# Performance work log

Measured on AMD Instinct MI355X. Metric: run time of the kernel, lower is better.

## Reference

```python
import jax, jax.numpy as jnp
import numpy as np

EMBED = 1024
HEADS = 16
DIM_HEAD = EMBED // HEADS
N, L = 4, 2048


def setup_inputs() -> dict:
    key = jax.random.key(0)
    ks = jax.random.split(key, 12)
    s = 0.02
    return {
        "q": jax.random.normal(ks[0], (N, L, EMBED), jnp.float32),
        "k": jax.random.normal(ks[1], (N, L, EMBED), jnp.float32),
        "v": jax.random.normal(ks[2], (N, L, EMBED), jnp.float32),
        "padding_mask": jnp.ones((N, L), dtype=bool),
        "sequence_mask": jnp.zeros((L, L), dtype=bool),
        # Linear(in, out): store weight as [out, in] like torch, bias [out]
        "Wq": jax.random.normal(ks[3], (EMBED, EMBED), jnp.float32) * s,
        "bq": jnp.zeros((EMBED,), jnp.float32),
        "Wk": jax.random.normal(ks[4], (EMBED, EMBED), jnp.float32) * s,
        "bk": jnp.zeros((EMBED,), jnp.float32),
        "Wv": jax.random.normal(ks[5], (EMBED, EMBED), jnp.float32) * s,
        "bv": jnp.zeros((EMBED,), jnp.float32),
        "Wo": jax.random.normal(ks[6], (EMBED, EMBED), jnp.float32) * s,
        "bo": jnp.zeros((EMBED,), jnp.float32),
    }


def reference(q, k, v, padding_mask, sequence_mask, Wq, bq, Wk, bk, Wv, bv, Wo, bo):
    n, lq, _ = q.shape
    lk = k.shape[1]
    # input projections
    qp = (q @ Wq.T + bq).reshape(n, lq, HEADS, DIM_HEAD)
    kp = (k @ Wk.T + bk).reshape(n, lk, HEADS, DIM_HEAD)
    vp = (v @ Wv.T + bv).reshape(n, lk, HEADS, DIM_HEAD)
    # energy: [n, h, lq, lk]
    energy = jnp.einsum('nqhd,nkhd->nhqk', qp, kp)
    attention = jax.nn.softmax(energy / jnp.sqrt(jnp.float32(EMBED)), axis=3)
    # NOTE: the original torch code calls masked_fill (non in-place) and
    # discards the result, so padding_mask / sequence_mask have NO effect.
    # Dropout is also never applied in forward. Replicated faithfully.
    out = jnp.einsum('nhqk,nkhd->nqhd', attention, vp)
    out = out.reshape(n, lq, EMBED)
    return out @ Wo.T + bo
```

## Files before the change

### kernel.cpp

```cpp
#include <hip/hip_runtime.h>
#include <stdint.h>

typedef _Float16 f16;
typedef _Float16 f16x8 __attribute__((ext_vector_type(8)));
typedef _Float16 f16x4 __attribute__((ext_vector_type(4)));
typedef _Float16 f16x2 __attribute__((ext_vector_type(2)));
typedef float f32x4 __attribute__((ext_vector_type(4)));

__device__ __forceinline__ f32x4 mfma16(f16x8 a, f16x8 b, f32x4 c) {
    return __builtin_amdgcn_mfma_f32_16x16x32_f16(a, b, c, 0, 0, 0);
}

__device__ __forceinline__ void gload16(const f16* g, f16* l) {
    __builtin_amdgcn_global_load_lds(
        (const __attribute__((address_space(1))) uint32_t*)g,
        (__attribute__((address_space(3))) uint32_t*)l, 16, 0, 0);
}

template <bool OUT16>
__device__ __forceinline__ void gemm_body(const f16* __restrict__ A,
                                          const f16* __restrict__ B,
                                          const float* __restrict__ bias,
                                          void* __restrict__ Cout, long ldo,
                                          int biasrow, float scale,
                                          long m0, long n0, f16* As, f16* Bs) {
    int tid = threadIdx.x;
    int lane = tid & 63, w = tid >> 6;
    int wm = w & 1, wn = w >> 1;
    int l15 = lane & 15, quad = lane >> 4;

    int r4 = lane >> 2;
    int c4 = (lane & 3) ^ ((lane >> 3) & 3);
    const f16* ag[2];
    const f16* bg[2];
    int off[2];
#pragma unroll
    for (int t = 0; t < 2; ++t) {
        int rb = t * 64 + w * 16;
        ag[t] = A + (m0 + rb + r4) * 1024 + c4 * 8;
        bg[t] = B + (n0 + rb + r4) * 1024 + c4 * 8;
        off[t] = rb * 32;
    }

    f32x4 acc[4][4] = {};

#pragma unroll
    for (int t = 0; t < 2; ++t) {
        gload16(ag[t], &As[off[t]]);
        gload16(bg[t], &Bs[off[t]]);
    }
#pragma unroll
    for (int t = 0; t < 2; ++t) {
        gload16(ag[t] + 32, &As[4096 + off[t]]);
        gload16(bg[t] + 32, &Bs[4096 + off[t]]);
    }
    asm volatile("s_waitcnt vmcnt(4)" ::: "memory");
    __builtin_amdgcn_s_barrier();
    __builtin_amdgcn_sched_barrier(0);

    int cur = 0;
    for (int kt = 0; kt < 32; ++kt) {
        if (kt < 30) {
            int slot = (cur == 0) ? 2 : cur - 1;
            const int ko = (kt + 2) * 32;
#pragma unroll
            for (int t = 0; t < 2; ++t) {
                gload16(ag[t] + ko, &As[slot * 4096 + off[t]]);
                gload16(bg[t] + ko, &Bs[slot * 4096 + off[t]]);
            }
        }
        const f16* as = As + cur * 4096;
        const f16* bs = Bs + cur * 4096;
        int cs = (quad ^ ((l15 >> 1) & 3)) * 8;
        f16x8 af[4], bf[4];
#pragma unroll
        for (int t = 0; t < 4; ++t) {
            af[t] = *(const f16x8*)&as[(wm * 64 + t * 16 + l15) * 32 + cs];
            bf[t] = *(const f16x8*)&bs[(wn * 64 + t * 16 + l15) * 32 + cs];
        }
#pragma unroll
        for (int i = 0; i < 4; ++i)
#pragma unroll
            for (int j = 0; j < 4; ++j)
                acc[i][j] = mfma16(af[i], bf[j], acc[i][j]);
        if (kt < 31) {
            if (kt < 30)
                asm volatile("s_waitcnt vmcnt(4)" ::: "memory");
            else
                asm volatile("s_waitcnt vmcnt(0)" ::: "memory");
            __builtin_amdgcn_s_barrier();
            __builtin_amdgcn_sched_barrier(0);
        }
        cur = (cur == 2) ? 0 : cur + 1;
    }

#pragma unroll
    for (int i = 0; i < 4; ++i) {
        int mrow = wm * 64 + i * 16 + quad * 4;
#pragma unroll
        for (int j = 0; j < 4; ++j) {
            int ncol = wn * 64 + j * 16 + l15;
            long gn = n0 + ncol;
#pragma unroll
            for (int r = 0; r < 4; ++r) {
                long gm = m0 + mrow + r;
                float v = (acc[i][j][r] + (biasrow ? bias[gm] : bias[gn])) * scale;
                if constexpr (OUT16)
                    ((f16*)Cout)[gm * ldo + gn] = (f16)v;
                else
                    ((float*)Cout)[gm * ldo + gn] = v;
            }
        }
    }
}

__global__ __launch_bounds__(256, 2) void qkv_proj(
    const f16* __restrict__ qh, const f16* __restrict__ kh,
    const f16* __restrict__ vh, const f16* __restrict__ Wh,
    const float* __restrict__ bq, const float* __restrict__ bk,
    const float* __restrict__ bv, f16* __restrict__ Qp, f16* __restrict__ Kp,
    f16* __restrict__ Vt) {
    __shared__ __align__(16) f16 As[3 * 128 * 32];
    __shared__ __align__(16) f16 Bs[3 * 128 * 32];
    int z = blockIdx.z;
    const f16* A;
    const f16* B;
    const float* bias;
    f16* C;
    long ldo;
    int biasrow;
    float scale;
    if (z == 0) {
        A = qh; B = Wh; bias = bq; C = Qp; ldo = 1024; biasrow = 0;
        scale = 0.0450842200277786f;
    } else if (z == 1) {
        A = kh; B = Wh + 1048576; bias = bk; C = Kp; ldo = 1024; biasrow = 0;
        scale = 1.0f;
    } else {
        A = Wh + 2097152; B = vh; bias = bv; C = Vt; ldo = 8192; biasrow = 1;
        scale = 1.0f;
    }
    long m0 = (long)(z == 2 ? blockIdx.y : blockIdx.x) * 128;
    long n0 = (long)(z == 2 ? blockIdx.x : blockIdx.y) * 128;
    gemm_body<true>(A, B, bias, C, ldo, biasrow, scale, m0, n0, As, Bs);
}

__global__ __launch_bounds__(256, 2) void o_proj(const f16* __restrict__ Op,
                                                 const f16* __restrict__ Wo,
                                                 const float* __restrict__ bo,
                                                 float* __restrict__ out) {
    __shared__ __align__(16) f16 As[3 * 128 * 32];
    __shared__ __align__(16) f16 Bs[3 * 128 * 32];
    gemm_body<false>(Op, Wo, bo, out, 1024, 0, 1.0f, (long)blockIdx.x * 128,
                     (long)blockIdx.y * 128, As, Bs);
}

__global__ __launch_bounds__(256, 2) void attn256(const f16* __restrict__ Qp,
                                                  const f16* __restrict__ Kp,
                                                  const f16* __restrict__ Vt,
                                                  f16* __restrict__ Op) {
    __shared__ __align__(16) f16 Ps0[128 * 64];
    __shared__ __align__(16) f16 Ps1[128 * 64];
    __shared__ __align__(16) f16 Ks[3][64 * 64];
    __shared__ __align__(16) f16 Vs[3][64 * 64];

    int tid = threadIdx.x;
    int lane = tid & 63, w = tid >> 6;
    int l15 = lane & 15, quad = lane >> 4;
    int b = blockIdx.x;
    int xcd = b & 7, slot = b >> 3;
    int nh = xcd * 8 + (slot >> 3);
    int qp = slot & 7;
    int nb = nh >> 4, h = nh & 15;
    long tok0 = (long)nb * 2048;
    long qrow0 = qp * 256;

    int rg = lane >> 3, cg = (lane & 7) ^ rg;

    const f16* qsrc0 = Qp + (tok0 + qrow0) * 1024 + h * 64;
    const f16* qsrc1 = qsrc0 + 128 * 1024;
#pragma unroll
    for (int t = 0; t < 4; ++t) {
        int rb = w * 32 + t * 8;
        gload16(qsrc0 + (rb + rg) * 1024 + cg * 8, &Ps0[rb * 64]);
        gload16(qsrc1 + (rb + rg) * 1024 + cg * 8, &Ps1[rb * 64]);
    }
    const f16* kptr = Kp + (tok0 + w * 16 + rg) * 1024 + h * 64 + cg * 8;
    const f16* vptr = Vt + ((long)h * 64 + w * 16 + rg) * 8192 + tok0 + cg * 8;
    gload16(kptr, &Ks[0][(w * 16) * 64]);
    gload16(kptr + 8 * 1024, &Ks[0][(w * 16 + 8) * 64]);
    gload16(vptr, &Vs[0][(w * 16) * 64]);
    gload16(vptr + (long)8 * 8192, &Vs[0][(w * 16 + 8) * 64]);
    gload16(kptr + 65536, &Ks[1][(w * 16) * 64]);
    gload16(kptr + 65536 + 8 * 1024, &Ks[1][(w * 16 + 8) * 64]);
    gload16(vptr + 64, &Vs[1][(w * 16) * 64]);
    gload16(vptr + 64 + (long)8 * 8192, &Vs[1][(w * 16 + 8) * 64]);
    const f16* kn = kptr + 2 * 65536;
    const f16* vn = vptr + 2 * 64;

    asm volatile("s_waitcnt vmcnt(8)" ::: "memory");
    f16x8 qf0[2][2], qf1[2][2];
#pragma unroll
    for (int ks = 0; ks < 2; ++ks) {
        int cc = (ks * 4 + quad) ^ (l15 & 7);
#pragma unroll
        for (int j = 0; j < 2; ++j) {
            qf0[ks][j] = *(const f16x8*)&Ps0[(w * 32 + j * 16 + l15) * 64 + cc * 8];
            qf1[ks][j] = *(const f16x8*)&Ps1[(w * 32 + j * 16 + l15) * 64 + cc * 8];
        }
    }
    asm volatile("s_waitcnt vmcnt(4)" ::: "memory");
    __builtin_amdgcn_s_barrier();
    __builtin_amdgcn_sched_barrier(0);

    f32x4 oacc0[2][4] = {}, oacc1[2][4] = {};
    float rs0[2] = {0.f, 0.f}, rs1[2] = {0.f, 0.f};
    const f32x4 z4 = {0.f, 0.f, 0.f, 0.f};

    int cur = 0;
    for (int kt = 0; kt < 32; ++kt) {
        f32x4 sacc0[4][2], sacc1[4][2];
        __builtin_amdgcn_s_setprio(1);
#pragma unroll
        for (int ks = 0; ks < 2; ++ks) {
            int cc = (ks * 4 + quad) ^ (l15 & 7);
            f16x8 a[4];
#pragma unroll
            for (int t = 0; t < 4; ++t)
                a[t] = *(const f16x8*)&Ks[cur][(t * 16 + l15) * 64 + cc * 8];
#pragma unroll
            for (int i = 0; i < 4; ++i)
#pragma unroll
                for (int j = 0; j < 2; ++j) {
                    if (ks == 0) {
                        sacc0[i][j] = mfma16(a[i], qf0[0][j], z4);
                        sacc1[i][j] = mfma16(a[i], qf1[0][j], z4);
                    } else {
                        sacc0[i][j] = mfma16(a[i], qf0[1][j], sacc0[i][j]);
                        sacc1[i][j] = mfma16(a[i], qf1[1][j], sacc1[i][j]);
                    }
                }
        }
        __builtin_amdgcn_s_setprio(0);
        if (kt < 30) {
            int nxt = (cur == 0) ? 2 : cur - 1;
            f16* kd = &Ks[nxt][(w * 16) * 64];
            f16* vd = &Vs[nxt][(w * 16) * 64];
            gload16(kn, kd);
            gload16(kn + 8 * 1024, kd + 8 * 64);
            gload16(vn, vd);
            gload16(vn + (long)8 * 8192, vd + 8 * 64);
            kn += 65536;
            vn += 64;
        }
#pragma unroll
        for (int i = 0; i < 4; ++i) {
#pragma unroll
            for (int j = 0; j < 2; ++j) {
                int qrow = w * 32 + j * 16 + l15;
                int kl = i * 16 + quad * 4;
                int c = kl >> 3;
                int off = qrow * 64 + ((c ^ (qrow & 7)) << 3) + (kl & 7);
                {
                    float p0 = __builtin_amdgcn_exp2f(sacc0[i][j][0]);
                    float p1 = __builtin_amdgcn_exp2f(sacc0[i][j][1]);
                    float p2 = __builtin_amdgcn_exp2f(sacc0[i][j][2]);
                    float p3 = __builtin_amdgcn_exp2f(sacc0[i][j][3]);
                    rs0[j] += (p0 + p1) + (p2 + p3);
                    f16x2 lo = __builtin_bit_cast(f16x2, __builtin_amdgcn_cvt_pkrtz(p0, p1));
                    f16x2 hi = __builtin_bit_cast(f16x2, __builtin_amdgcn_cvt_pkrtz(p2, p3));
                    f16x4 ph;
                    ph[0] = lo[0]; ph[1] = lo[1]; ph[2] = hi[0]; ph[3] = hi[1];
                    *(f16x4*)&Ps0[off] = ph;
                }
                {
                    float p0 = __builtin_amdgcn_exp2f(sacc1[i][j][0]);
                    float p1 = __builtin_amdgcn_exp2f(sacc1[i][j][1]);
                    float p2 = __builtin_amdgcn_exp2f(sacc1[i][j][2]);
                    float p3 = __builtin_amdgcn_exp2f(sacc1[i][j][3]);
                    rs1[j] += (p0 + p1) + (p2 + p3);
                    f16x2 lo = __builtin_bit_cast(f16x2, __builtin_amdgcn_cvt_pkrtz(p0, p1));
                    f16x2 hi = __builtin_bit_cast(f16x2, __builtin_amdgcn_cvt_pkrtz(p2, p3));
                    f16x4 ph;
                    ph[0] = lo[0]; ph[1] = lo[1]; ph[2] = hi[0]; ph[3] = hi[1];
                    *(f16x4*)&Ps1[off] = ph;
                }
            }
        }
        __builtin_amdgcn_s_setprio(1);
#pragma unroll
        for (int ks = 0; ks < 2; ++ks) {
            int cc = (ks * 4 + quad) ^ (l15 & 7);
            f16x8 bf[4];
#pragma unroll
            for (int j = 0; j < 4; ++j)
                bf[j] = *(const f16x8*)&Vs[cur][(j * 16 + l15) * 64 + cc * 8];
            f16x8 af0[2], af1[2];
#pragma unroll
            for (int i = 0; i < 2; ++i) {
                af0[i] = *(const f16x8*)&Ps0[(w * 32 + i * 16 + l15) * 64 + cc * 8];
                af1[i] = *(const f16x8*)&Ps1[(w * 32 + i * 16 + l15) * 64 + cc * 8];
            }
#pragma unroll
            for (int i = 0; i < 2; ++i)
#pragma unroll
                for (int j = 0; j < 4; ++j) {
                    oacc0[i][j] = mfma16(af0[i], bf[ks * 0 + j], oacc0[i][j]);
                    oacc1[i][j] = mfma16(af1[i], bf[j], oacc1[i][j]);
                }
        }
        __builtin_amdgcn_s_setprio(0);
        if (kt < 31) {
            if (kt < 30)
                asm volatile("s_waitcnt vmcnt(4)" ::: "memory");
            else
                asm volatile("s_waitcnt vmcnt(0)" ::: "memory");
            __builtin_amdgcn_s_barrier();
            __builtin_amdgcn_sched_barrier(0);
        }
        cur = (cur == 2) ? 0 : cur + 1;
    }

    float* lsi = (float*)&Ks[0][0];
#pragma unroll
    for (int j = 0; j < 2; ++j) {
        rs0[j] += __shfl_xor(rs0[j], 16, 64);
        rs0[j] += __shfl_xor(rs0[j], 32, 64);
        rs1[j] += __shfl_xor(rs1[j], 16, 64);
        rs1[j] += __shfl_xor(rs1[j], 32, 64);
    }
    if (lane < 16) {
        lsi[w * 32 + lane] = 1.0f / rs0[0];
        lsi[w * 32 + 16 + lane] = 1.0f / rs0[1];
        lsi[128 + w * 32 + lane] = 1.0f / rs1[0];
        lsi[128 + w * 32 + 16 + lane] = 1.0f / rs1[1];
    }

    long otok = tok0 + qrow0;
#pragma unroll
    for (int i = 0; i < 2; ++i) {
        int qrow = w * 32 + i * 16 + quad * 4;
#pragma unroll
        for (int j = 0; j < 4; ++j) {
            int d = j * 16 + l15;
#pragma unroll
            for (int r = 0; r < 4; ++r) {
                Op[(otok + qrow + r) * 1024 + h * 64 + d] =
                    (f16)(oacc0[i][j][r] * lsi[qrow + r]);
                Op[(otok + 128 + qrow + r) * 1024 + h * 64 + d] =
                    (f16)(oacc1[i][j][r] * lsi[128 + qrow + r]);
            }
        }
    }
}

__global__ void cvt_all(const float* __restrict__ q, const float* __restrict__ k,
                        const float* __restrict__ v, const float* __restrict__ w0,
                        const float* __restrict__ w1, const float* __restrict__ w2,
                        const float* __restrict__ w3, f16* __restrict__ qh,
                        f16* __restrict__ kh, f16* __restrict__ vh,
                        f16* __restrict__ wh) {
    long id = (long)blockIdx.x * 256 + threadIdx.x;
    const float* s;
    f16* d;
    long off;
    if (id < 3145728) {
        int which = (int)(id >> 20);
        off = (id & 1048575) * 8;
        s = which == 0 ? q : which == 1 ? k : v;
        d = which == 0 ? qh : which == 1 ? kh : vh;
    } else {
        long id2 = id - 3145728;
        int wi = (int)(id2 >> 17);
        off = (id2 & 131071) * 8;
        s = wi == 0 ? w0 : wi == 1 ? w1 : wi == 2 ? w2 : w3;
        d = wh + (long)wi * 1048576;
    }
    f32x4 a = *(const f32x4*)(s + off);
    f32x4 b = *(const f32x4*)(s + off + 4);
    f16x8 hv;
    hv[0] = (f16)a[0]; hv[1] = (f16)a[1]; hv[2] = (f16)a[2]; hv[3] = (f16)a[3];
    hv[4] = (f16)b[0]; hv[5] = (f16)b[1]; hv[6] = (f16)b[2]; hv[7] = (f16)b[3];
    *(f16x8*)(d + off) = hv;
}

extern "C" void kernel_launch(void* const* d_in, const int* in_sizes, int n_in,
                              void* d_out, int out_size, void* d_ws, size_t ws_size,
                              hipStream_t stream) {
    const float* q  = (const float*)d_in[0];
    const float* k  = (const float*)d_in[1];
    const float* v  = (const float*)d_in[2];
    const float* Wq = (const float*)d_in[5];
    const float* bq = (const float*)d_in[6];
    const float* Wk = (const float*)d_in[7];
    const float* bk = (const float*)d_in[8];
    const float* Wv = (const float*)d_in[9];
    const float* bv = (const float*)d_in[10];
    const float* Wo = (const float*)d_in[11];
    const float* bo = (const float*)d_in[12];

    char* ws = (char*)d_ws;
    f16* qh = (f16*)ws;
    f16* kh = (f16*)(ws + (16L << 20));
    f16* vh = (f16*)(ws + (32L << 20));
    f16* Wh = (f16*)(ws + (48L << 20));
    f16* Qp = (f16*)(ws + (56L << 20));
    f16* Kp = (f16*)(ws + (72L << 20));
    f16* Vt = (f16*)(ws + (88L << 20));
    f16* Op = (f16*)(ws + (104L << 20));

    cvt_all<<<14336, 256, 0, stream>>>(q, k, v, Wq, Wk, Wv, Wo, qh, kh, vh, Wh);

    qkv_proj<<<dim3(64, 8, 3), 256, 0, stream>>>(qh, kh, vh, Wh, bq, bk, bv,
                                                 Qp, Kp, Vt);

    attn256<<<512, 256, 0, stream>>>(Qp, Kp, Vt, Op);

    o_proj<<<dim3(64, 8), 256, 0, stream>>>(Op, Wh + 3145728, bo, (float*)d_out);
}
```

Measured before the change: 340.5 us.

## Switch projection GEMMs to 256x128 tiles with 8 waves and 64-wide K steps

Replaces the 128x128, 4-wave, triple-buffered GEMM body with a 256x128 tile computed by 8 waves. Each K step is now 64 wide and double-buffered, with next-tile loads split across two half-steps and MFMA blocks raised to higher priority. The aim is more operand reuse per LDS byte and fewer barriers per K. In exchange, LDS per block grows to about 96KB, which likely allows only one block per CU and gives coarser grid balance (768 and 256 blocks). It also drops a no-op index expression in the attention kernel.

```diff
diff --git a/kernel.cpp b/kernel.cpp
--- a/kernel.cpp
+++ b/kernel.cpp
@@ -18,80 +18,88 @@
 }
 
 template <bool OUT16>
-__device__ __forceinline__ void gemm_body(const f16* __restrict__ A,
-                                          const f16* __restrict__ B,
-                                          const float* __restrict__ bias,
-                                          void* __restrict__ Cout, long ldo,
-                                          int biasrow, float scale,
-                                          long m0, long n0, f16* As, f16* Bs) {
+__device__ __forceinline__ void gemm256(const f16* __restrict__ A,
+                                        const f16* __restrict__ B,
+                                        const float* __restrict__ bias,
+                                        void* __restrict__ Cout, long ldo,
+                                        int biasrow, float scale,
+                                        long m0, long n0, f16* As, f16* Bs) {
     int tid = threadIdx.x;
     int lane = tid & 63, w = tid >> 6;
-    int wm = w & 1, wn = w >> 1;
+    int wm = w >> 1, wn = w & 1;
     int l15 = lane & 15, quad = lane >> 4;
-
-    int r4 = lane >> 2;
-    int c4 = (lane & 3) ^ ((lane >> 3) & 3);
-    const f16* ag[2];
-    const f16* bg[2];
-    int off[2];
-#pragma unroll
-    for (int t = 0; t < 2; ++t) {
-        int rb = t * 64 + w * 16;
-        ag[t] = A + (m0 + rb + r4) * 1024 + c4 * 8;
-        bg[t] = B + (n0 + rb + r4) * 1024 + c4 * 8;
-        off[t] = rb * 32;
-    }
+    int rg = lane >> 3, cg = (lane & 7) ^ rg;
+
+    const f16* srcA = A + (m0 + w * 8 + rg) * 1024 + cg * 8;
+    const f16* srcB = B + (n0 + w * 8 + rg) * 1024 + cg * 8;
+    f16* dA = As + w * 512;
+    f16* dB = Bs + w * 512;
 
     f32x4 acc[4][4] = {};
 
 #pragma unroll
-    for (int t = 0; t < 2; ++t) {
-        gload16(ag[t], &As[off[t]]);
-        gload16(bg[t], &Bs[off[t]]);
-    }
-#pragma unroll
-    for (int t = 0; t < 2; ++t) {
-        gload16(ag[t] + 32, &As[4096 + off[t]]);
-        gload16(bg[t] + 32, &Bs[4096 + off[t]]);
-    }
-    asm volatile("s_waitcnt vmcnt(4)" ::: "memory");
+    for (int p = 0; p < 4; ++p) gload16(srcA + p * 65536, dA + p * 4096);
+#pragma unroll
+    for (int p = 0; p < 2; ++p) gload16(srcB + p * 65536, dB + p * 4096);
+    asm volatile("s_waitcnt vmcnt(0)" ::: "memory");
     __builtin_amdgcn_s_barrier();
     __builtin_amdgcn_sched_barrier(0);
 
-    int cur = 0;
-    for (int kt = 0; kt < 32; ++kt) {
-        if (kt < 30) {
-            int slot = (cur == 0) ? 2 : cur - 1;
-            const int ko = (kt + 2) * 32;
-#pragma unroll
-            for (int t = 0; t < 2; ++t) {
-                gload16(ag[t] + ko, &As[slot * 4096 + off[t]]);
-                gload16(bg[t] + ko, &Bs[slot * 4096 + off[t]]);
-            }
-        }
-        const f16* as = As + cur * 4096;
-        const f16* bs = Bs + cur * 4096;
-        int cs = (quad ^ ((l15 >> 1) & 3)) * 8;
-        f16x8 af[4], bf[4];
-#pragma unroll
-        for (int t = 0; t < 4; ++t) {
-            af[t] = *(const f16x8*)&as[(wm * 64 + t * 16 + l15) * 32 + cs];
-            bf[t] = *(const f16x8*)&bs[(wn * 64 + t * 16 + l15) * 32 + cs];
-        }
-#pragma unroll
-        for (int i = 0; i < 4; ++i)
-#pragma unroll
-            for (int j = 0; j < 4; ++j)
-                acc[i][j] = mfma16(af[i], bf[j], acc[i][j]);
-        if (kt < 31) {
-            if (kt < 30)
-                asm volatile("s_waitcnt vmcnt(4)" ::: "memory");
-            else
-                asm volatile("s_waitcnt vmcnt(0)" ::: "memory");
-            __builtin_amdgcn_s_barrier();
-            __builtin_amdgcn_sched_barrier(0);
-        }
-        cur = (cur == 2) ? 0 : cur + 1;
+    for (int kt = 0; kt < 16; ++kt) {
+        int c = kt & 1;
+        const f16* as = As + c * 16384;
+        const f16* bs = Bs + c * 8192;
+        f16* an = dA + (c ^ 1) * 16384;
+        f16* bn = dB + (c ^ 1) * 8192;
+        long ko = (long)(kt + 1) * 64;
+
+        if (kt < 15) {
+            gload16(srcA + ko, an);
+            gload16(srcA + 65536 + ko, an + 4096);
+            gload16(srcB + ko, bn);
+        }
+        {
+            int cc8 = (quad ^ (l15 & 7)) * 8;
+            f16x8 af[4], bf[4];
+#pragma unroll
+            for (int t = 0; t < 4; ++t) {
+                af[t] = *(const f16x8*)&as[(wm * 64 + t * 16 + l15) * 64 + cc8];
+                bf[t] = *(const f16x8*)&bs[(wn * 64 + t * 16 + l15) * 64 + cc8];
+            }
+            __builtin_amdgcn_s_setprio(1);
+#pragma unroll
+            for (int i = 0; i < 4; ++i)
+#pragma unroll
+                for (int j = 0; j < 4; ++j)
+                    acc[i][j] = mfma16(af[i], bf[j], acc[i][j]);
+            __builtin_amdgcn_s_setprio(0);
+        }
+        __builtin_amdgcn_s_barrier();
+
+        if (kt < 15) {
+            gload16(srcA + 2 * 65536 + ko, an + 8192);
+            gload16(srcA + 3 * 65536 + ko, an + 12288);
+            gload16(srcB + 65536 + ko, bn + 4096);
+        }
+        {
+            int cc8 = ((4 + quad) ^ (l15 & 7)) * 8;
+            f16x8 af[4], bf[4];
+#pragma unroll
+            for (int t = 0; t < 4; ++t) {
+                af[t] = *(const f16x8*)&as[(wm * 64 + t * 16 + l15) * 64 + cc8];
+                bf[t] = *(const f16x8*)&bs[(wn * 64 + t * 16 + l15) * 64 + cc8];
+            }
+            __builtin_amdgcn_s_setprio(1);
+#pragma unroll
+            for (int i = 0; i < 4; ++i)
+#pragma unroll
+                for (int j = 0; j < 4; ++j)
+                    acc[i][j] = mfma16(af[i], bf[j], acc[i][j]);
+            __builtin_amdgcn_s_setprio(0);
+        }
+        if (kt < 15) asm volatile("s_waitcnt vmcnt(0)" ::: "memory");
+        __builtin_amdgcn_s_barrier();
+        __builtin_amdgcn_sched_barrier(0);
     }
 
 #pragma unroll
@@ -114,15 +122,16 @@
     }
 }
 
-__global__ __launch_bounds__(256, 2) void qkv_proj(
+__global__ __launch_bounds__(512, 2) void qkv_proj(
     const f16* __restrict__ qh, const f16* __restrict__ kh,
     const f16* __restrict__ vh, const f16* __restrict__ Wh,
     const float* __restrict__ bq, const float* __restrict__ bk,
     const float* __restrict__ bv, f16* __restrict__ Qp, f16* __restrict__ Kp,
     f16* __restrict__ Vt) {
-    __shared__ __align__(16) f16 As[3 * 128 * 32];
-    __shared__ __align__(16) f16 Bs[3 * 128 * 32];
-    int z = blockIdx.z;
+    __shared__ __align__(16) f16 As[2 * 256 * 64];
+    __shared__ __align__(16) f16 Bs[2 * 128 * 64];
+    int z = blockIdx.y;
+    int flat = blockIdx.x;
     const f16* A;
     const f16* B;
     const float* bias;
@@ -140,19 +149,27 @@
         A = Wh + 2097152; B = vh; bias = bv; C = Vt; ldo = 8192; biasrow = 1;
         scale = 1.0f;
     }
-    long m0 = (long)(z == 2 ? blockIdx.y : blockIdx.x) * 128;
-    long n0 = (long)(z == 2 ? blockIdx.x : blockIdx.y) * 128;
-    gemm_body<true>(A, B, bias, C, ldo, biasrow, scale, m0, n0, As, Bs);
-}
-
-__global__ __launch_bounds__(256, 2) void o_proj(const f16* __restrict__ Op,
+    long m0, n0;
+    if (z == 2) {
+        m0 = (long)(flat & 3) * 256;
+        n0 = (long)(flat >> 2) * 128;
+    } else {
+        m0 = (long)(flat & 31) * 256;
+        n0 = (long)(flat >> 5) * 128;
+    }
+    gemm256<true>(A, B, bias, C, ldo, biasrow, scale, m0, n0, As, Bs);
+}
+
+__global__ __launch_bounds__(512, 2) void o_proj(const f16* __restrict__ Op,
                                                  const f16* __restrict__ Wo,
                                                  const float* __restrict__ bo,
                                                  float* __restrict__ out) {
-    __shared__ __align__(16) f16 As[3 * 128 * 32];
-    __shared__ __align__(16) f16 Bs[3 * 128 * 32];
-    gemm_body<false>(Op, Wo, bo, out, 1024, 0, 1.0f, (long)blockIdx.x * 128,
-                     (long)blockIdx.y * 128, As, Bs);
+    __shared__ __align__(16) f16 As[2 * 256 * 64];
+    __shared__ __align__(16) f16 Bs[2 * 128 * 64];
+    int flat = blockIdx.x;
+    long m0 = (long)(flat & 31) * 256;
+    long n0 = (long)(flat >> 5) * 128;
+    gemm256<false>(Op, Wo, bo, out, 1024, 0, 1.0f, m0, n0, As, Bs);
 }
 
 __global__ __launch_bounds__(256, 2) void attn256(const f16* __restrict__ Qp,
@@ -305,7 +322,7 @@
             for (int i = 0; i < 2; ++i)
 #pragma unroll
                 for (int j = 0; j < 4; ++j) {
-                    oacc0[i][j] = mfma16(af0[i], bf[ks * 0 + j], oacc0[i][j]);
+                    oacc0[i][j] = mfma16(af0[i], bf[j], oacc0[i][j]);
                     oacc1[i][j] = mfma16(af1[i], bf[j], oacc1[i][j]);
                 }
         }
@@ -411,10 +428,10 @@
 
     cvt_all<<<14336, 256, 0, stream>>>(q, k, v, Wq, Wk, Wv, Wo, qh, kh, vh, Wh);
 
-    qkv_proj<<<dim3(64, 8, 3), 256, 0, stream>>>(qh, kh, vh, Wh, bq, bk, bv,
-                                                 Qp, Kp, Vt);
+    qkv_proj<<<dim3(256, 3), 512, 0, stream>>>(qh, kh, vh, Wh, bq, bk, bv,
+                                               Qp, Kp, Vt);
 
     attn256<<<512, 256, 0, stream>>>(Qp, Kp, Vt, Op);
 
-    o_proj<<<dim3(64, 8), 256, 0, stream>>>(Op, Wh + 3145728, bo, (float*)d_out);
-}
+    o_proj<<<256, 512, 0, stream>>>(Op, Wh + 3145728, bo, (float*)d_out);
+}
```

Result: slower. 362.0 us (+6.3%).

## Fuse fp32-to-fp16 conversion into projection GEMM tile loads, drop cvt kernel

Applied to the files above, without the earlier changes.

Removes the standalone conversion kernel that wrote fp16 copies of the inputs and weights. The QKV and output projection GEMMs now load fp32 tiles into registers, convert them to fp16 and store them to LDS, using a two-stage double buffer instead of the three-stage async global-to-LDS pipeline. This avoids a full extra read-and-write pass over the activations and one launch. In exchange, GEMM tile loads move twice the bytes and go through registers, which can weaken latency hiding. MFMA priority hints are also added.

```diff
diff --git a/kernel.cpp b/kernel.cpp
--- a/kernel.cpp
+++ b/kernel.cpp
@@ -17,56 +17,85 @@
         (__attribute__((address_space(3))) uint32_t*)l, 16, 0, 0);
 }
 
-template <bool OUT16>
-__device__ __forceinline__ void gemm_body(const f16* __restrict__ A,
-                                          const f16* __restrict__ B,
-                                          const float* __restrict__ bias,
-                                          void* __restrict__ Cout, long ldo,
-                                          int biasrow, float scale,
-                                          long m0, long n0, f16* As, f16* Bs) {
+__device__ __forceinline__ f16x8 cvt8(f32x4 a, f32x4 b) {
+    f16x8 h;
+    h[0] = (f16)a[0]; h[1] = (f16)a[1]; h[2] = (f16)a[2]; h[3] = (f16)a[3];
+    h[4] = (f16)b[0]; h[5] = (f16)b[1]; h[6] = (f16)b[2]; h[7] = (f16)b[3];
+    return h;
+}
+
+template <bool A16, bool OUT16>
+__device__ __forceinline__ void gemm_fused(const void* __restrict__ Av,
+                                           const float* __restrict__ B,
+                                           const float* __restrict__ bias,
+                                           void* __restrict__ Cout, long ldo,
+                                           int biasrow, float scale,
+                                           long m0, long n0, f16* As, f16* Bs) {
     int tid = threadIdx.x;
     int lane = tid & 63, w = tid >> 6;
     int wm = w & 1, wn = w >> 1;
     int l15 = lane & 15, quad = lane >> 4;
 
     int r4 = lane >> 2;
+    int g = lane & 3;
+    int sc = g ^ ((r4 >> 1) & 3);
     int c4 = (lane & 3) ^ ((lane >> 3) & 3);
-    const f16* ag[2];
-    const f16* bg[2];
-    int off[2];
+
+    const f16* a16 = (const f16*)Av;
+    const float* a32 = (const float*)Av;
+
+    const f16* a16src[2];
+    const float* a32src[2];
+    const float* b32src[2];
+    int lwoff[2];
 #pragma unroll
     for (int t = 0; t < 2; ++t) {
-        int rb = t * 64 + w * 16;
-        ag[t] = A + (m0 + rb + r4) * 1024 + c4 * 8;
-        bg[t] = B + (n0 + rb + r4) * 1024 + c4 * 8;
-        off[t] = rb * 32;
-    }
+        long row = t * 64 + w * 16 + r4;
+        if constexpr (A16)
+            a16src[t] = a16 + (m0 + row) * 1024 + c4 * 8;
+        else
+            a32src[t] = a32 + (m0 + row) * 1024 + g * 8;
+        b32src[t] = B + (n0 + row) * 1024 + g * 8;
+        lwoff[t] = t * 2048 + w * 512;
+    }
+    int wroff = r4 * 32 + sc * 8;
 
     f32x4 acc[4][4] = {};
 
 #pragma unroll
     for (int t = 0; t < 2; ++t) {
-        gload16(ag[t], &As[off[t]]);
-        gload16(bg[t], &Bs[off[t]]);
-    }
-#pragma unroll
-    for (int t = 0; t < 2; ++t) {
-        gload16(ag[t] + 32, &As[4096 + off[t]]);
-        gload16(bg[t] + 32, &Bs[4096 + off[t]]);
-    }
-    asm volatile("s_waitcnt vmcnt(4)" ::: "memory");
+        if constexpr (A16) {
+            gload16(a16src[t], As + lwoff[t]);
+        } else {
+            f32x4 x0 = *(const f32x4*)(a32src[t]);
+            f32x4 x1 = *(const f32x4*)(a32src[t] + 4);
+            *(f16x8*)&As[lwoff[t] + wroff] = cvt8(x0, x1);
+        }
+        f32x4 y0 = *(const f32x4*)(b32src[t]);
+        f32x4 y1 = *(const f32x4*)(b32src[t] + 4);
+        *(f16x8*)&Bs[lwoff[t] + wroff] = cvt8(y0, y1);
+    }
+    if constexpr (A16) asm volatile("s_waitcnt vmcnt(0)" ::: "memory");
+    asm volatile("s_waitcnt lgkmcnt(0)" ::: "memory");
     __builtin_amdgcn_s_barrier();
     __builtin_amdgcn_sched_barrier(0);
 
-    int cur = 0;
     for (int kt = 0; kt < 32; ++kt) {
-        if (kt < 30) {
-            int slot = (cur == 0) ? 2 : cur - 1;
-            const int ko = (kt + 2) * 32;
+        int cur = kt & 1;
+        int nxt = cur ^ 1;
+        f32x4 la[2][2], lb[2][2];
+        if (kt < 31) {
+            long ko = (long)(kt + 1) * 32;
 #pragma unroll
             for (int t = 0; t < 2; ++t) {
-                gload16(ag[t] + ko, &As[slot * 4096 + off[t]]);
-                gload16(bg[t] + ko, &Bs[slot * 4096 + off[t]]);
+                if constexpr (A16) {
+                    gload16(a16src[t] + ko, As + nxt * 4096 + lwoff[t]);
+                } else {
+                    la[t][0] = *(const f32x4*)(a32src[t] + ko);
+                    la[t][1] = *(const f32x4*)(a32src[t] + ko + 4);
+                }
+                lb[t][0] = *(const f32x4*)(b32src[t] + ko);
+                lb[t][1] = *(const f32x4*)(b32src[t] + ko + 4);
             }
         }
         const f16* as = As + cur * 4096;
@@ -78,20 +107,27 @@
             af[t] = *(const f16x8*)&as[(wm * 64 + t * 16 + l15) * 32 + cs];
             bf[t] = *(const f16x8*)&bs[(wn * 64 + t * 16 + l15) * 32 + cs];
         }
+        __builtin_amdgcn_s_setprio(1);
 #pragma unroll
         for (int i = 0; i < 4; ++i)
 #pragma unroll
             for (int j = 0; j < 4; ++j)
                 acc[i][j] = mfma16(af[i], bf[j], acc[i][j]);
+        __builtin_amdgcn_s_setprio(0);
         if (kt < 31) {
-            if (kt < 30)
-                asm volatile("s_waitcnt vmcnt(4)" ::: "memory");
-            else
-                asm volatile("s_waitcnt vmcnt(0)" ::: "memory");
+#pragma unroll
+            for (int t = 0; t < 2; ++t) {
+                if constexpr (!A16)
+                    *(f16x8*)&As[nxt * 4096 + lwoff[t] + wroff] =
+                        cvt8(la[t][0], la[t][1]);
+                *(f16x8*)&Bs[nxt * 4096 + lwoff[t] + wroff] =
+                    cvt8(lb[t][0], lb[t][1]);
+            }
+            if constexpr (A16) asm volatile("s_waitcnt vmcnt(0)" ::: "memory");
+            asm volatile("s_waitcnt lgkmcnt(0)" ::: "memory");
             __builtin_amdgcn_s_barrier();
             __builtin_amdgcn_sched_barrier(0);
         }
-        cur = (cur == 2) ? 0 : cur + 1;
     }
 
 #pragma unroll
@@ -115,44 +151,46 @@
 }
 
 __global__ __launch_bounds__(256, 2) void qkv_proj(
-    const f16* __restrict__ qh, const f16* __restrict__ kh,
-    const f16* __restrict__ vh, const f16* __restrict__ Wh,
+    const float* __restrict__ q, const float* __restrict__ k,
+    const float* __restrict__ v, const float* __restrict__ Wq,
+    const float* __restrict__ Wk, const float* __restrict__ Wv,
     const float* __restrict__ bq, const float* __restrict__ bk,
     const float* __restrict__ bv, f16* __restrict__ Qp, f16* __restrict__ Kp,
     f16* __restrict__ Vt) {
-    __shared__ __align__(16) f16 As[3 * 128 * 32];
-    __shared__ __align__(16) f16 Bs[3 * 128 * 32];
+    __shared__ __align__(16) f16 As[2 * 4096];
+    __shared__ __align__(16) f16 Bs[2 * 4096];
     int z = blockIdx.z;
-    const f16* A;
-    const f16* B;
+    const float* A;
+    const float* B;
     const float* bias;
     f16* C;
     long ldo;
     int biasrow;
     float scale;
     if (z == 0) {
-        A = qh; B = Wh; bias = bq; C = Qp; ldo = 1024; biasrow = 0;
+        A = q; B = Wq; bias = bq; C = Qp; ldo = 1024; biasrow = 0;
         scale = 0.0450842200277786f;
     } else if (z == 1) {
-        A = kh; B = Wh + 1048576; bias = bk; C = Kp; ldo = 1024; biasrow = 0;
+        A = k; B = Wk; bias = bk; C = Kp; ldo = 1024; biasrow = 0;
         scale = 1.0f;
     } else {
-        A = Wh + 2097152; B = vh; bias = bv; C = Vt; ldo = 8192; biasrow = 1;
+        A = Wv; B = v; bias = bv; C = Vt; ldo = 8192; biasrow = 1;
         scale = 1.0f;
     }
     long m0 = (long)(z == 2 ? blockIdx.y : blockIdx.x) * 128;
     long n0 = (long)(z == 2 ? blockIdx.x : blockIdx.y) * 128;
-    gemm_body<true>(A, B, bias, C, ldo, biasrow, scale, m0, n0, As, Bs);
+    gemm_fused<false, true>(A, B, bias, C, ldo, biasrow, scale, m0, n0, As, Bs);
 }
 
 __global__ __launch_bounds__(256, 2) void o_proj(const f16* __restrict__ Op,
-                                                 const f16* __restrict__ Wo,
+                                                 const float* __restrict__ Wo,
                                                  const float* __restrict__ bo,
                                                  float* __restrict__ out) {
-    __shared__ __align__(16) f16 As[3 * 128 * 32];
-    __shared__ __align__(16) f16 Bs[3 * 128 * 32];
-    gemm_body<false>(Op, Wo, bo, out, 1024, 0, 1.0f, (long)blockIdx.x * 128,
-                     (long)blockIdx.y * 128, As, Bs);
+    __shared__ __align__(16) f16 As[2 * 4096];
+    __shared__ __align__(16) f16 Bs[2 * 4096];
+    gemm_fused<true, false>(Op, Wo, bo, out, 1024, 0, 1.0f,
+                            (long)blockIdx.x * 128, (long)blockIdx.y * 128,
+                            As, Bs);
 }
 
 __global__ __launch_bounds__(256, 2) void attn256(const f16* __restrict__ Qp,
@@ -305,7 +343,7 @@
             for (int i = 0; i < 2; ++i)
 #pragma unroll
                 for (int j = 0; j < 4; ++j) {
-                    oacc0[i][j] = mfma16(af0[i], bf[ks * 0 + j], oacc0[i][j]);
+                    oacc0[i][j] = mfma16(af0[i], bf[j], oacc0[i][j]);
                     oacc1[i][j] = mfma16(af1[i], bf[j], oacc1[i][j]);
                 }
         }
@@ -352,36 +390,6 @@
             }
         }
     }
-}
-
-__global__ void cvt_all(const float* __restrict__ q, const float* __restrict__ k,
-                        const float* __restrict__ v, const float* __restrict__ w0,
-                        const float* __restrict__ w1, const float* __restrict__ w2,
-                        const float* __restrict__ w3, f16* __restrict__ qh,
-                        f16* __restrict__ kh, f16* __restrict__ vh,
-                        f16* __restrict__ wh) {
-    long id = (long)blockIdx.x * 256 + threadIdx.x;
-    const float* s;
-    f16* d;
-    long off;
-    if (id < 3145728) {
-        int which = (int)(id >> 20);
-        off = (id & 1048575) * 8;
-        s = which == 0 ? q : which == 1 ? k : v;
-        d = which == 0 ? qh : which == 1 ? kh : vh;
-    } else {
-        long id2 = id - 3145728;
-        int wi = (int)(id2 >> 17);
-        off = (id2 & 131071) * 8;
-        s = wi == 0 ? w0 : wi == 1 ? w1 : wi == 2 ? w2 : w3;
-        d = wh + (long)wi * 1048576;
-    }
-    f32x4 a = *(const f32x4*)(s + off);
-    f32x4 b = *(const f32x4*)(s + off + 4);
-    f16x8 hv;
-    hv[0] = (f16)a[0]; hv[1] = (f16)a[1]; hv[2] = (f16)a[2]; hv[3] = (f16)a[3];
-    hv[4] = (f16)b[0]; hv[5] = (f16)b[1]; hv[6] = (f16)b[2]; hv[7] = (f16)b[3];
-    *(f16x8*)(d + off) = hv;
 }
 
 extern "C" void kernel_launch(void* const* d_in, const int* in_sizes, int n_in,
@@ -400,21 +408,15 @@
     const float* bo = (const float*)d_in[12];
 
     char* ws = (char*)d_ws;
-    f16* qh = (f16*)ws;
-    f16* kh = (f16*)(ws + (16L << 20));
-    f16* vh = (f16*)(ws + (32L << 20));
-    f16* Wh = (f16*)(ws + (48L << 20));
-    f16* Qp = (f16*)(ws + (56L << 20));
-    f16* Kp = (f16*)(ws + (72L << 20));
-    f16* Vt = (f16*)(ws + (88L << 20));
-    f16* Op = (f16*)(ws + (104L << 20));
-
-    cvt_all<<<14336, 256, 0, stream>>>(q, k, v, Wq, Wk, Wv, Wo, qh, kh, vh, Wh);
-
-    qkv_proj<<<dim3(64, 8, 3), 256, 0, stream>>>(qh, kh, vh, Wh, bq, bk, bv,
-                                                 Qp, Kp, Vt);
+    f16* Qp = (f16*)ws;
+    f16* Kp = (f16*)(ws + (16L << 20));
+    f16* Vt = (f16*)(ws + (32L << 20));
+    f16* Op = (f16*)(ws + (48L << 20));
+
+    qkv_proj<<<dim3(64, 8, 3), 256, 0, stream>>>(q, k, v, Wq, Wk, Wv,
+                                                 bq, bk, bv, Qp, Kp, Vt);
 
     attn256<<<512, 256, 0, stream>>>(Qp, Kp, Vt, Op);
 
-    o_proj<<<dim3(64, 8), 256, 0, stream>>>(Op, Wh + 3145728, bo, (float*)d_out);
-}
+    o_proj<<<dim3(64, 8), 256, 0, stream>>>(Op, Wo, bo, (float*)d_out);
+}
```

New measurement: 358.8 us. +5.4%, slower.
